# Performance work log

Measured on AMD Instinct MI355X. Metric: run time of the kernel, lower is better.

The kernel has to match this reference:

```python
import jax, jax.numpy as jnp
import numpy as np

B, H, CS, HF = 128, 32, 1, 64  # batch, heads, decode chunk (=1 token), head_dim


def setup_inputs() -> dict:
    key = jax.random.key(0)
    k1, k2, k3, k4, k5, k6 = jax.random.split(key, 6)
    return {
        "W1_init": jax.random.normal(k1, (B, H, HF, HF), dtype=jnp.float32) * 0.02,
        "W1_grad": jax.random.normal(k2, (B, H, HF, HF), dtype=jnp.float32) * 0.02,
        "XA": jax.random.normal(k3, (B, H, CS, HF), dtype=jnp.float32),
        "XB": jax.random.normal(k4, (B, H, CS, HF), dtype=jnp.float32),
        "XC": jax.random.normal(k5, (B, H, CS, HF), dtype=jnp.float32),
        "coeff": jax.random.uniform(k6, (B, H, CS, 1), dtype=jnp.float32) * 0.01,
    }


def reference(W1_init, W1_grad, XA, XB, XC, coeff):
    """TTT-M1 fast-weight decode step (one gradient-descent update per (b,h)).

    Mirrors _m1_decode_kernel with CS=1:
      Z1          = XB @ W1_init - XA                 # inner-loop prediction error
      W1_grad    += XB^T outer Z1                     # accumulate fast-weight grad
      W1_init    -= coeff * W1_grad                   # SGD step on fast weights
      Out         = XC @ W1_init                      # query the updated weights
    Returns (Out, W1_init_new, W1_grad_new).
    """
    # [B,H,CS,HF] @ [B,H,HF,HF] -> [B,H,CS,HF]
    Z1 = jnp.einsum('bhcf,bhfd->bhcd', XB, W1_init) - XA
    # outer product XB^T Z1 summed over the CS axis -> [B,H,HF,HF]
    W1_grad_new = W1_grad + jnp.einsum('bhcf,bhcd->bhfd', XB, Z1)
    # coeff: [B,H,CS,1] -> broadcast as per-(b,h) scalar (CS=1) over [HF,HF]
    W1_init_new = W1_init - coeff[..., 0:1] * W1_grad_new
    Out = jnp.einsum('bhcf,bhfd->bhcd', XC, W1_init_new)
    return Out, W1_init_new, W1_grad_new
```

## Files before the change

### kernel.cpp

```cpp
#include <hip/hip_runtime.h>
#include <hip/hip_bf16.h>


namespace {

constexpr int HFD = 64;

union F4 { float4 v; float f[4]; };

__global__ __launch_bounds__(256, 4) void ttt_m1_decode(
    const float* __restrict__ W1i,
    const float* __restrict__ W1g,
    const float* __restrict__ XA,
    const float* __restrict__ XB,
    const float* __restrict__ XC,
    const float* __restrict__ coeff,
    float* __restrict__ oOut,
    float* __restrict__ oW1,
    float* __restrict__ oG)
{
    const int bh  = blockIdx.x;
    const int tid = threadIdx.x;
    const int c   = tid & 15;
    const int r   = tid >> 4;
    const int d0  = c << 2;
    const int f0  = r << 2;

    const size_t mbase = (size_t)bh * (HFD * HFD);
    const float* Wi = W1i + mbase;
    const float* Wg = W1g + mbase;
    const float* xa = XA + bh * HFD;
    const float* xb = XB + bh * HFD;
    const float* xc = XC + bh * HFD;
    const float cf  = coeff[bh];

    __shared__ float redZ[16][HFD];
    __shared__ float redO[16][HFD];

    F4 wi[4], wg[4];
#pragma unroll
    for (int j = 0; j < 4; ++j) {
        wi[j].v = *reinterpret_cast<const float4*>(Wi + (f0 + j) * HFD + d0);
        wg[j].v = *reinterpret_cast<const float4*>(Wg + (f0 + j) * HFD + d0);
    }
    float xbv[4], xcv[4];
#pragma unroll
    for (int j = 0; j < 4; ++j) { xbv[j] = xb[f0 + j]; xcv[j] = xc[f0 + j]; }
    F4 xav; xav.v = *reinterpret_cast<const float4*>(xa + d0);

    F4 zp;
#pragma unroll
    for (int k = 0; k < 4; ++k)
        zp.f[k] = xbv[0]*wi[0].f[k] + xbv[1]*wi[1].f[k]
                + xbv[2]*wi[2].f[k] + xbv[3]*wi[3].f[k];
    *reinterpret_cast<float4*>(&redZ[r][d0]) = zp.v;
    __syncthreads();

    F4 z1; z1.v = make_float4(0.f, 0.f, 0.f, 0.f);
#pragma unroll
    for (int rp = 0; rp < 16; ++rp) {
        F4 t; t.v = *reinterpret_cast<const float4*>(&redZ[rp][d0]);
#pragma unroll
        for (int k = 0; k < 4; ++k) z1.f[k] += t.f[k];
    }
#pragma unroll
    for (int k = 0; k < 4; ++k) z1.f[k] -= xav.f[k];

    F4 op; op.v = make_float4(0.f, 0.f, 0.f, 0.f);
#pragma unroll
    for (int j = 0; j < 4; ++j) {
        F4 wout, gout;
#pragma unroll
        for (int k = 0; k < 4; ++k) {
            float gn = wg[j].f[k] + xbv[j] * z1.f[k];
            float wn = wi[j].f[k] - cf * gn;
            op.f[k] += xcv[j] * wn;
            gout.f[k] = gn;
            wout.f[k] = wn;
        }
        const size_t off = mbase + (size_t)(f0 + j) * HFD + d0;
        *reinterpret_cast<float4*>(oW1 + off) = wout.v;
        *reinterpret_cast<float4*>(oG  + off) = gout.v;
    }

    *reinterpret_cast<float4*>(&redO[r][d0]) = op.v;
    __syncthreads();

    if (tid < HFD) {
        float s = 0.f;
#pragma unroll
        for (int rp = 0; rp < 16; ++rp) s += redO[rp][tid];
        oOut[bh * HFD + tid] = s;
    }
}

}

extern "C" void kernel_launch(void* const* d_in, const int* in_sizes, int n_in,
                              void* d_out, int out_size, void* d_ws, size_t ws_size,
                              hipStream_t stream) {
    const float* W1i = (const float*)d_in[0];
    const float* W1g = (const float*)d_in[1];
    const float* XA  = (const float*)d_in[2];
    const float* XB  = (const float*)d_in[3];
    const float* XC  = (const float*)d_in[4];
    const float* cf  = (const float*)d_in[5];

    const int BH = in_sizes[0] / (64 * 64);

    float* out  = (float*)d_out;
    float* oOut = out;
    float* oW1  = out + (size_t)BH * 64;
    float* oG   = oW1 + (size_t)BH * 4096;

    ttt_m1_decode<<<BH, 256, 0, stream>>>(W1i, W1g, XA, XB, XC, cf, oOut, oW1, oG);
}
```

Measured before the change: 46.53 us.

## Map one wavefront per head matrix with shuffle reductions and nontemporal stores

Each 64-lane wavefront now handles one (b,h) matrix, with four matrices per block. Reductions use cross-lane xor shuffles instead of shared memory and __syncthreads, and W1_grad is loaded lazily in the second pass. Output stores are nontemporal to avoid polluting cache. Each lane now holds 16 float4 rows in registers, which raises register pressure and gives fewer blocks, and the launch assumes BH is divisible by 4.

```diff
diff --git a/kernel.cpp b/kernel.cpp
--- a/kernel.cpp
+++ b/kernel.cpp
@@ -6,9 +6,9 @@
 
 constexpr int HFD = 64;
 
-union F4 { float4 v; float f[4]; };
+typedef float f32x4 __attribute__((ext_vector_type(4)));
 
-__global__ __launch_bounds__(256, 4) void ttt_m1_decode(
+__global__ __launch_bounds__(256, 4) void ttt_m1_decode_wave(
     const float* __restrict__ W1i,
     const float* __restrict__ W1g,
     const float* __restrict__ XA,
@@ -19,12 +19,12 @@
     float* __restrict__ oW1,
     float* __restrict__ oG)
 {
-    const int bh  = blockIdx.x;
-    const int tid = threadIdx.x;
-    const int c   = tid & 15;
-    const int r   = tid >> 4;
-    const int d0  = c << 2;
-    const int f0  = r << 2;
+    const int tid  = threadIdx.x;
+    const int wave = tid >> 6;
+    const int lane = tid & 63;
+    const int bh   = blockIdx.x * 4 + wave;
+    const int fg   = lane >> 4;
+    const int d0   = (lane & 15) << 2;
 
     const size_t mbase = (size_t)bh * (HFD * HFD);
     const float* Wi = W1i + mbase;
@@ -34,64 +34,43 @@
     const float* xc = XC + bh * HFD;
     const float cf  = coeff[bh];
 
-    __shared__ float redZ[16][HFD];
-    __shared__ float redO[16][HFD];
-
-    F4 wi[4], wg[4];
+    f32x4 w[16];
+    f32x4 z = (f32x4)0.f;
 #pragma unroll
-    for (int j = 0; j < 4; ++j) {
-        wi[j].v = *reinterpret_cast<const float4*>(Wi + (f0 + j) * HFD + d0);
-        wg[j].v = *reinterpret_cast<const float4*>(Wg + (f0 + j) * HFD + d0);
-    }
-    float xbv[4], xcv[4];
-#pragma unroll
-    for (int j = 0; j < 4; ++j) { xbv[j] = xb[f0 + j]; xcv[j] = xc[f0 + j]; }
-    F4 xav; xav.v = *reinterpret_cast<const float4*>(xa + d0);
-
-    F4 zp;
-#pragma unroll
-    for (int k = 0; k < 4; ++k)
-        zp.f[k] = xbv[0]*wi[0].f[k] + xbv[1]*wi[1].f[k]
-                + xbv[2]*wi[2].f[k] + xbv[3]*wi[3].f[k];
-    *reinterpret_cast<float4*>(&redZ[r][d0]) = zp.v;
-    __syncthreads();
-
-    F4 z1; z1.v = make_float4(0.f, 0.f, 0.f, 0.f);
-#pragma unroll
-    for (int rp = 0; rp < 16; ++rp) {
-        F4 t; t.v = *reinterpret_cast<const float4*>(&redZ[rp][d0]);
-#pragma unroll
-        for (int k = 0; k < 4; ++k) z1.f[k] += t.f[k];
+    for (int j = 0; j < 16; ++j) {
+        const int f = fg * 16 + j;
+        w[j] = *reinterpret_cast<const f32x4*>(Wi + f * HFD + d0);
+        const float xbf = xb[f];
+        z += xbf * w[j];
     }
 #pragma unroll
-    for (int k = 0; k < 4; ++k) z1.f[k] -= xav.f[k];
+    for (int k = 0; k < 4; ++k) {
+        z[k] += __shfl_xor(z[k], 16, 64);
+        z[k] += __shfl_xor(z[k], 32, 64);
+    }
+    z -= *reinterpret_cast<const f32x4*>(xa + d0);
 
-    F4 op; op.v = make_float4(0.f, 0.f, 0.f, 0.f);
+    f32x4 o = (f32x4)0.f;
 #pragma unroll
-    for (int j = 0; j < 4; ++j) {
-        F4 wout, gout;
+    for (int j = 0; j < 16; ++j) {
+        const int f = fg * 16 + j;
+        f32x4 g = *reinterpret_cast<const f32x4*>(Wg + f * HFD + d0);
+        const float xbf = xb[f];
+        const float xcf = xc[f];
+        f32x4 gn = g + xbf * z;
+        f32x4 wn = w[j] - cf * gn;
+        o += xcf * wn;
+        const size_t off = mbase + (size_t)f * HFD + d0;
+        __builtin_nontemporal_store(gn, reinterpret_cast<f32x4*>(oG  + off));
+        __builtin_nontemporal_store(wn, reinterpret_cast<f32x4*>(oW1 + off));
+    }
 #pragma unroll
-        for (int k = 0; k < 4; ++k) {
-            float gn = wg[j].f[k] + xbv[j] * z1.f[k];
-            float wn = wi[j].f[k] - cf * gn;
-            op.f[k] += xcv[j] * wn;
-            gout.f[k] = gn;
-            wout.f[k] = wn;
-        }
-        const size_t off = mbase + (size_t)(f0 + j) * HFD + d0;
-        *reinterpret_cast<float4*>(oW1 + off) = wout.v;
-        *reinterpret_cast<float4*>(oG  + off) = gout.v;
+    for (int k = 0; k < 4; ++k) {
+        o[k] += __shfl_xor(o[k], 16, 64);
+        o[k] += __shfl_xor(o[k], 32, 64);
     }
-
-    *reinterpret_cast<float4*>(&redO[r][d0]) = op.v;
-    __syncthreads();
-
-    if (tid < HFD) {
-        float s = 0.f;
-#pragma unroll
-        for (int rp = 0; rp < 16; ++rp) s += redO[rp][tid];
-        oOut[bh * HFD + tid] = s;
-    }
+    if (fg == 0)
+        *reinterpret_cast<f32x4*>(oOut + bh * HFD + d0) = o;
 }
 
 }
@@ -113,5 +92,6 @@
     float* oW1  = out + (size_t)BH * 64;
     float* oG   = oW1 + (size_t)BH * 4096;
 
-    ttt_m1_decode<<<BH, 256, 0, stream>>>(W1i, W1g, XA, XB, XC, cf, oOut, oW1, oG);
+    ttt_m1_decode_wave<<<BH / 4, 256, 0, stream>>>(W1i, W1g, XA, XB, XC, cf,
+                                                   oOut, oW1, oG);
 }
```

After: 72.98 us. +56.8%, slower.
